# Performance work log

Measured on AMD Instinct MI355X. Metric: run time of the kernel, lower is better.

The kernel has to match this reference:

```python
import jax, jax.numpy as jnp
import numpy as np

N = 16384
C_IN = 128
C_OUT = 128
S_DIM = 4
P_DIM = 32
K = 16


def setup_inputs() -> dict:
    key = jax.random.key(0)
    ks = jax.random.split(key, 8)
    lim = lambda fan_in: 1.0 / np.sqrt(fan_in)
    u = lambda k_, shape, b: jax.random.uniform(k_, shape, jnp.float32, -b, b)
    return {
        "x": jax.random.normal(ks[0], (N, C_IN), jnp.float32),
        "Ws": u(ks[1], (S_DIM, C_IN), lim(C_IN)),
        "bs": u(ks[2], (S_DIM,), lim(C_IN)),
        "Wh": u(ks[3], (P_DIM, C_IN), lim(C_IN)),
        "bh": u(ks[4], (P_DIM,), lim(C_IN)),
        "W1": u(ks[5], (C_OUT, C_IN), lim(C_IN)),
        "W2": u(ks[6], (C_OUT, 2 * P_DIM), lim(2 * P_DIM)),
        "b2": u(ks[7], (C_OUT,), lim(2 * P_DIM)),
        "k": K,
    }


def reference(x, Ws, bs, Wh, bh, W1, W2, b2, k):
    # latent space positions and message vectors
    s = x @ Ws.T + bs            # [N, S]
    h = x @ Wh.T + bh            # [N, P]
    # squared-distance matrix via Gram trick (monotone in true distance,
    # so k-NN indices match torch.cdist + topk(largest=False))
    sq = jnp.sum(s * s, axis=-1)                         # [N]
    d2 = sq[:, None] + sq[None, :] - 2.0 * (s @ s.T)     # [N, N]
    _, idx = jax.lax.top_k(-d2, k)                       # [N, k] neighbour ids (incl. self)
    # exact squared latent distance to selected neighbours (as in torch code)
    s_j = s[idx]                                          # [N, k, S]
    w = jnp.exp(-10.0 * jnp.sum((s[:, None, :] - s_j) ** 2, axis=-1))  # [N, k]
    msg = h[idx] * w[..., None]                           # [N, k, P]
    agg = jnp.concatenate([msg.mean(axis=1), msg.max(axis=1)], axis=-1)  # [N, 2P]
    return x @ W1.T + agg @ W2.T + b2                     # [N, C_OUT]
```

## Files before the change

kernel.cpp:

```cpp
#include <hip/hip_runtime.h>
#include <hip/hip_bf16.h>


#define NPTS 16384
#define CIN  128
#define SD   4
#define PD   32
#define KNN  16
#define COUT 128
#define FLTMAX 3.4028234663852886e+38f
#define NBIN 33
#define QPB  8
#define QCAP 512
#define MCAP 128
#define EPAD 1e-3f

typedef float v2f __attribute__((ext_vector_type(2)));
typedef unsigned int uint;
typedef unsigned long long u64;
typedef unsigned short u16;
typedef __attribute__((ext_vector_type(8))) short bf16x8;
typedef __attribute__((ext_vector_type(4))) float f32x4;
typedef __attribute__((ext_vector_type(16))) float f32x16;

#define WS_S4     0
#define WS_H      0x40000
#define WS_AGG_M  0x280000
#define WS_SA     0x280000
#define WS_SB     0x300000
#define WS_WT_M   0x680000
#define WS_T2     0x6A0000
#define WS_MASK   0x700000
#define WS_NEED_M 0x2700000
#define WS_CJ_F   0x400000
#define WS_AGG_F  0xC00000
#define WS_WT_F   0x1000000
#define JS   16
#define TJF  (NPTS/JS)

__device__ __forceinline__ float d2f(const float4 a, const float4 b) {
  v2f d0 = {a.x - b.x, a.y - b.y};
  v2f d1 = {a.z - b.z, a.w - b.w};
  v2f pr = d0*d0 + d1*d1;
  return pr.x + pr.y;
}

__device__ __forceinline__ u16 f2bf(float x) {
  uint u = __float_as_uint(x);
  uint r = (u + 0x7FFFu + ((u >> 16) & 1u)) >> 16;
  return (u16)r;
}
__device__ __forceinline__ float bf2f(u16 h) {
  return __uint_as_float(((uint)h) << 16);
}

__global__ __launch_bounds__(256) void k1_proj(
    const float* __restrict__ x, const float* __restrict__ Ws, const float* __restrict__ bs,
    const float* __restrict__ Wh, const float* __restrict__ bh,
    float4* __restrict__ s4, float* __restrict__ h) {
  __shared__ float  lw[36*128];
  __shared__ float  lx[64*132];
  __shared__ double rs[3*64*5];
  __shared__ float  rh[3*64*33];
  const int t = threadIdx.x;
  const int row0 = blockIdx.x * 64;
  for (int i2 = t; i2 < 36*128; i2 += 256)
    lw[i2] = (i2 < 512) ? Ws[i2] : Wh[i2 - 512];
#pragma unroll
  for (int g = 0; g < 8; ++g) {
    int fi = g*256 + t;
    int r = fi >> 5, c4 = fi & 31;
    *(float4*)&lx[r*132 + c4*4] = *(const float4*)&x[(size_t)(row0 + r)*CIN + c4*4];
  }
  __syncthreads();
  const int kq = t >> 6;
  const int r  = t & 63;
  const int kb = kq * 32;
  double sacc[4] = {0.0, 0.0, 0.0, 0.0};
  float  hacc[32];
#pragma unroll
  for (int p = 0; p < 32; ++p) hacc[p] = 0.f;
#pragma unroll
  for (int k4 = 0; k4 < 8; ++k4) {
    float4 xv = *(const float4*)&lx[r*132 + kb + k4*4];
    int kg = kb + k4*4;
#pragma unroll
    for (int p = 0; p < 4; ++p) {
      float4 wv = *(const float4*)&lw[p*128 + kg];
      sacc[p] = fma((double)xv.x, (double)wv.x, sacc[p]);
      sacc[p] = fma((double)xv.y, (double)wv.y, sacc[p]);
      sacc[p] = fma((double)xv.z, (double)wv.z, sacc[p]);
      sacc[p] = fma((double)xv.w, (double)wv.w, sacc[p]);
    }
#pragma unroll
    for (int p = 0; p < 32; ++p) {
      float4 wv = *(const float4*)&lw[(4+p)*128 + kg];
      hacc[p] = fmaf(xv.x, wv.x, fmaf(xv.y, wv.y, fmaf(xv.z, wv.z, fmaf(xv.w, wv.w, hacc[p]))));
    }
  }
  if (kq > 0) {
    const int bq = kq - 1;
#pragma unroll
    for (int d = 0; d < 4; ++d) rs[(bq*64 + r)*5 + d] = sacc[d];
#pragma unroll
    for (int p = 0; p < 32; ++p) rh[(bq*64 + r)*33 + p] = hacc[p];
  }
  __syncthreads();
  if (kq == 0) {
    const int row = row0 + r;
    float so[4];
#pragma unroll
    for (int d = 0; d < 4; ++d) {
      double sd = sacc[d] + rs[(0*64 + r)*5 + d] + rs[(1*64 + r)*5 + d]
                + rs[(2*64 + r)*5 + d] + (double)bs[d];
      so[d] = (float)sd;
    }
    s4[row] = make_float4(so[0], so[1], so[2], so[3]);
#pragma unroll
    for (int p4 = 0; p4 < 8; ++p4) {
      float o[4];
#pragma unroll
      for (int c = 0; c < 4; ++c) {
        int p = p4*4 + c;
        o[c] = hacc[p] + rh[(0*64 + r)*33 + p] + rh[(1*64 + r)*33 + p]
             + rh[(2*64 + r)*33 + p] + bh[p];
      }
      *(float4*)&h[(size_t)row*PD + p4*4] = make_float4(o[0], o[1], o[2], o[3]);
    }
  }
}

__global__ __launch_bounds__(256) void k2t_thresh(
    const float4* __restrict__ s4, float* __restrict__ t2) {
  __shared__ float4 tile[2064];
  __shared__ uint   lhist[256*NBIN];
  const int t = threadIdx.x;
#pragma unroll
  for (int g = 0; g < 8; ++g) {
    int j = g*256 + t;
    tile[j + (j >> 7)] = s4[j];
  }
#pragma unroll
  for (int b = 0; b < NBIN; ++b) lhist[t*NBIN + b] = 0u;
  const int ql = t >> 4, tq = t & 15;
  const int q  = blockIdx.x*16 + ql;
  const float4 sq = s4[q];
  __syncthreads();
  float tau = d2f(sq, tile[tq*129]);
#pragma unroll
  for (int m = 1; m < 16; m <<= 1) tau = fmaxf(tau, __shfl_xor(tau, m, 16));
  const int ktop = (int)(__float_as_uint(tau) >> 21);
  const int hb = t*NBIN;
#pragma unroll 4
  for (int u = 0; u < 128; ++u) {
    float4 p = tile[tq*129 + u];
    float e = d2f(sq, p);
    int key = (int)(__float_as_uint(e) >> 21);
    int rel = ktop - key;
    rel = rel < 0 ? 0 : (rel > 32 ? 32 : rel);
    atomicAdd(&lhist[hb + rel], 1u);
  }
  __syncthreads();
  uint c0 = 0, c1 = 0;
  const int qb = ql*16;
  for (int u = 0; u < 16; ++u) {
    c0 += lhist[(qb + u)*NBIN + tq*2];
    c1 += (tq*2 + 1 < NBIN) ? lhist[(qb + u)*NBIN + tq*2 + 1] : 0u;
  }
  int S = (int)(c0 + c1);
#pragma unroll
  for (int d = 1; d < 16; d <<= 1) {
    int v = __shfl_down(S, d, 16);
    S += (tq + d < 16) ? v : 0;
  }
  int g = -1;
  if (S >= KNN) g = 2*tq;
  if (S - (int)c0 >= KNN) g = 2*tq + 1;
#pragma unroll
  for (int m = 1; m < 16; m <<= 1) g = max(g, __shfl_xor(g, m, 16));
  if (tq == 0) {
    uint K = (uint)(ktop - g);
    t2[q] = __uint_as_float((K << 21) | 0x1FFFFFu);
  }
}

__global__ __launch_bounds__(256) void k1b_pack(
    const float4* __restrict__ s4, const float* __restrict__ t2,
    uint4* __restrict__ sA, uint4* __restrict__ sB) {
  const int i = blockIdx.x*256 + threadIdx.x;
  const float4 s = s4[i];
  float sv[4] = {s.x, s.y, s.z, s.w};
  const float n2 = s.x*s.x + s.y*s.y + s.z*s.z + s.w*s.w;
  u16 hb[4], lb[4];
#pragma unroll
  for (int d = 0; d < 4; ++d) {
    u16 hh = f2bf(sv[d]);
    hb[d] = hh;
    lb[d] = f2bf(sv[d] - bf2f(hh));
  }
  const float aq = -0.5f*(n2 - t2[i]) + EPAD;
  const float bn = -0.5f*n2;
  u16 aqh = f2bf(aq); u16 aql = f2bf(aq - bf2f(aqh));
  u16 bnh = f2bf(bn); u16 bnl = f2bf(bn - bf2f(bnh));
  const uint oneone = 0x3F803F80u;
  uint a0 = (uint)hb[0] | ((uint)hb[1] << 16);
  uint a1 = (uint)hb[2] | ((uint)hb[3] << 16);
  uint l0 = (uint)lb[0] | ((uint)lb[1] << 16);
  uint l1 = (uint)lb[2] | ((uint)lb[3] << 16);
  uint aqw = (uint)aqh | ((uint)aql << 16);
  uint bnw = (uint)bnh | ((uint)bnl << 16);
  uint4 A0; A0.x = a0; A0.y = a1; A0.z = a0; A0.w = a1;
  uint4 A1; A1.x = l0; A1.y = l1; A1.z = oneone; A1.w = aqw;
  uint4 B0; B0.x = a0; B0.y = a1; B0.z = l0; B0.w = l1;
  uint4 B1; B1.x = a0; B1.y = a1; B1.z = bnw; B1.w = oneone;
  sA[(size_t)i*2]     = A0;
  sA[(size_t)i*2 + 1] = A1;
  sB[(size_t)i*2]     = B0;
  sB[(size_t)i*2 + 1] = B1;
}

__device__ __forceinline__ uint packbits16(const f32x16 a, const int shft) {
  uint b[4];
#pragma unroll
  for (int g = 0; g < 4; ++g) {
    uint bg = 0u;
#pragma unroll
    for (int e = 3; e >= 0; --e)
      bg = bg + bg + ((~__float_as_uint(a[4*g + e])) >> 31);
    b[g] = bg;
  }
  return (b[0] | (b[1] << 8) | (b[2] << 16) | (b[3] << 24)) << shft;
}

__global__ __launch_bounds__(256) void k2b_mfma(
    const u16* __restrict__ sA, const u16* __restrict__ sB, uint4* __restrict__ maskw) {
  __shared__ u16 lB[1024*16];
  const int t   = threadIdx.x;
  const int wv  = t >> 6, ln = t & 63;
  const int l31 = ln & 31, hi = ln >> 5;
  const int qbase = (blockIdx.x >> 4) * 256 + wv * 64;
  const int j0    = (blockIdx.x & 15) * 1024;
  for (int r = t; r < 1024; r += 256) {
    const uint4* src = (const uint4*)&sB[(size_t)(j0 + r)*16];
    uint4 v0 = src[0], v1 = src[1];
    *(uint4*)&lB[r*16]     = v0;
    *(uint4*)&lB[r*16 + 8] = v1;
  }
  const bf16x8 qf0 = *(const bf16x8*)&sA[(size_t)(qbase + l31)*16 + hi*8];
  const bf16x8 qf1 = *(const bf16x8*)&sA[(size_t)(qbase + 32 + l31)*16 + hi*8];
  __syncthreads();
  const int sh = hi * 4;
  const f32x16 zc = {0.f,0.f,0.f,0.f,0.f,0.f,0.f,0.f,0.f,0.f,0.f,0.f,0.f,0.f,0.f,0.f};
#pragma unroll 1
  for (int cc = 0; cc < 8; ++cc) {
    uint w0[4], w1[4];
#pragma unroll
    for (int jt = 0; jt < 4; ++jt) {
      const bf16x8 af = *(const bf16x8*)&lB[(cc*128 + jt*32 + l31)*16 + hi*8];
      f32x16 a0 = __builtin_amdgcn_mfma_f32_32x32x16_bf16(af, qf0, zc, 0, 0, 0);
      f32x16 a1 = __builtin_amdgcn_mfma_f32_32x32x16_bf16(af, qf1, zc, 0, 0, 0);
      w0[jt] = packbits16(a0, sh);
      w1[jt] = packbits16(a1, sh);
    }
    uint of[4];
#pragma unroll
    for (int jt = 0; jt < 4; ++jt) {
      uint f0 = w0[jt] | (uint)__shfl_xor((int)w0[jt], 32);
      uint f1 = w1[jt] | (uint)__shfl_xor((int)w1[jt], 32);
      of[jt] = hi ? f1 : f0;
    }
    const int c = (blockIdx.x & 15)*8 + cc;
    uint4 o; o.x = of[0]; o.y = of[1]; o.z = of[2]; o.w = of[3];
    maskw[(size_t)c*NPTS + qbase + ln] = o;
  }
}

__global__ __launch_bounds__(256) void k3_sel2(
    const float4* __restrict__ s4, const float* __restrict__ h,
    const uint4* __restrict__ maskw, float* __restrict__ agg) {
  __shared__ u64  qbuf[QPB*MCAP];
  __shared__ u64  keys[QPB*QCAP];
  __shared__ u64  win[QPB*KNN];
  __shared__ uint hist[QPB*32];
  __shared__ uint cnts[QPB];
  __shared__ uint mc[QPB];
  unsigned short* jl = (unsigned short*)qbuf;
  const int t  = threadIdx.x;
  const int ql = t >> 5, ln = t & 31;
  const int q  = blockIdx.x*QPB + ql;
  if (ln == 0) { cnts[ql] = 0u; mc[ql] = 0u; }
  hist[ql*32 + ln] = 0u;
  if (ln < KNN) win[ql*KNN + ln] = 0ull;
  const float4 sq = s4[q];
  __syncthreads();
  const int qa = t & 7;
  const int cg = t >> 3;
  uint wv[16]; int pc = 0;
#pragma unroll
  for (int u = 0; u < 4; ++u) {
    const int c = cg + u*32;
    uint4 m4 = maskw[(size_t)c*NPTS + blockIdx.x*QPB + qa];
    wv[u*4+0] = m4.x; wv[u*4+1] = m4.y; wv[u*4+2] = m4.z; wv[u*4+3] = m4.w;
    pc += __popc(m4.x) + __popc(m4.y) + __popc(m4.z) + __popc(m4.w);
  }
  int base = (int)atomicAdd(&cnts[qa], (uint)pc);
#pragma unroll
  for (int w = 0; w < 16; ++w) {
    uint bits = wv[w];
    const int jb = (cg + (w >> 2)*32)*128 + (w & 3)*32;
    while (bits) {
      int b = __builtin_ctz(bits); bits &= bits - 1;
      if (base < QCAP) jl[qa*QCAP + base] = (unsigned short)(jb + b);
      ++base;
    }
  }
  __syncthreads();
  const int cnt = min((int)cnts[ql], QCAP);
  uint kmax = 0u;
  for (int u = ln; u < cnt; u += 32) {
    int j = jl[ql*QCAP + u];
    float e = d2f(sq, s4[j]);
    uint db = __float_as_uint(e);
    keys[ql*QCAP + u] = ((u64)db << 14) | (uint)j;
    kmax = max(kmax, db >> 21);
  }
#pragma unroll
  for (int m = 1; m < 32; m <<= 1) kmax = max(kmax, (uint)__shfl_xor((int)kmax, m, 32));
  for (int u = ln; u < cnt; u += 32) {
    uint cls = (uint)(keys[ql*QCAP + u] >> 35);
    uint rel = min(kmax - cls, 31u);
    atomicAdd(&hist[ql*32 + rel], 1u);
  }
  __syncthreads();
  uint cum = hist[ql*32 + ln];
#pragma unroll
  for (int d = 1; d < 32; d <<= 1) {
    uint v = (uint)__shfl_down((int)cum, d, 32);
    if (ln + d < 32) cum += v;
  }
  const uint need = (uint)(cnt < KNN ? cnt : KNN);
  u64 bal = __ballot(cum >= need);
  uint half = (uint)(bal >> (((t >> 5) & 1) * 32));
  const uint rstar = 31u - (uint)__builtin_clz(half);
  const uint bcls = kmax - rstar;
  __syncthreads();
  for (int u = ln; u < cnt; u += 32) {
    u64 key = keys[ql*QCAP + u];
    if ((uint)(key >> 35) <= bcls) {
      uint pos = atomicAdd(&mc[ql], 1u);
      if (pos < MCAP) qbuf[ql*MCAP + pos] = key;
    }
  }
  __syncthreads();
  const int mcnt = (int)mc[ql];
  if (mcnt <= MCAP) {
    for (int w = ln; w < mcnt; w += 32) {
      u64 key = qbuf[ql*MCAP + w];
      int rank = 0;
      for (int v = 0; v < mcnt; ++v) rank += (qbuf[ql*MCAP + v] < key) ? 1 : 0;
      if (rank < KNN) win[ql*KNN + rank] = key;
    }
  } else {
    for (int u = ln; u < cnt; u += 32) {
      u64 key = keys[ql*QCAP + u];
      if ((uint)(key >> 35) <= bcls) {
        int rank = 0;
        for (int v = 0; v < cnt; ++v) rank += (keys[ql*QCAP + v] < key) ? 1 : 0;
        if (rank < KNN) win[ql*KNN + rank] = key;
      }
    }
  }
  __syncthreads();
  float sum = 0.f, mx = -FLTMAX;
#pragma unroll 1
  for (int r = 0; r < KNN; ++r) {
    u64 key = win[ql*KNN + r];
    float d2 = __uint_as_float((uint)(key >> 14));
    int j = (int)(key & 16383u);
    float w = __expf(-10.f * d2);
    float m = w * h[(size_t)j*PD + ln];
    sum += m; mx = fmaxf(mx, m);
  }
  agg[(size_t)q*64 + ln]      = sum * 0.0625f;
  agg[(size_t)q*64 + 32 + ln] = mx;
}

__global__ __launch_bounds__(256) void k2_knn_fb(
    const float4* __restrict__ s4, unsigned short* __restrict__ cand_j) {
  __shared__ float4 tile[TJF];
  __shared__ int    lbuf[256*33];
  const int t  = threadIdx.x;
  const int ib = blockIdx.x & 31;
  const int jc = blockIdx.x >> 5;
  const int jbase = jc * TJF;
#pragma unroll
  for (int g = 0; g < 4; ++g) tile[g*256 + t] = s4[jbase + g*256 + t];
  const int ia = ib*256 + t;
  const int ic = ia + 8192;
  const float4 sa = s4[ia];
  const float4 sc = s4[ic];
  __syncthreads();
  float va[KNN], vb[KNN]; int ja[KNN], jb[KNN];
#pragma unroll
  for (int q = 0; q < KNN; ++q) { va[q] = FLTMAX; ja[q] = 0; vb[q] = FLTMAX; jb[q] = 0; }
  float cma = FLTMAX, cmb = FLTMAX;
  int cpa = 0, cpb = 0, ca = 0, cb = 0;
  auto insertA = [&](float e, int jj) {
#pragma unroll
    for (int q = 0; q < KNN; ++q) if (q == cpa) { va[q] = e; ja[q] = jj; }
    cma = va[0]; cpa = 0;
#pragma unroll
    for (int q = 1; q < KNN; ++q) { if (va[q] > cma) { cma = va[q]; cpa = q; } }
  };
  auto insertB = [&](float e, int jj) {
#pragma unroll
    for (int q = 0; q < KNN; ++q) if (q == cpb) { vb[q] = e; jb[q] = jj; }
    cmb = vb[0]; cpb = 0;
#pragma unroll
    for (int q = 1; q < KNN; ++q) { if (vb[q] > cmb) { cmb = vb[q]; cpb = q; } }
  };
  auto compactA = [&]() {
    for (int u = 0; u < ca; ++u) {
      int jj = lbuf[t*33 + u];
      float e = d2f(sa, tile[jj]);
      if (e < cma) insertA(e, jj);
    }
    ca = 0;
  };
  auto compactB = [&]() {
    for (int u = 0; u < cb; ++u) {
      int jj = lbuf[t*33 + 16 + u];
      float e = d2f(sc, tile[jj]);
      if (e < cmb) insertB(e, jj);
    }
    cb = 0;
  };
  for (int ob = 0; ob < TJF/8; ++ob) {
#pragma unroll
    for (int u = 0; u < 8; ++u) {
      int jj = ob*8 + u;
      float4 p = tile[jj];
      float ea = d2f(sa, p);
      float eb = d2f(sc, p);
      if (ea < cma) { lbuf[t*33 + ca] = jj; ++ca; }
      if (eb < cmb) { lbuf[t*33 + 16 + cb] = jj; ++cb; }
    }
    if (__any(ca > 8)) compactA();
    if (__any(cb > 8)) compactB();
  }
  compactA(); compactB();
#pragma unroll
  for (int q = 0; q < KNN; ++q) {
    int c = jc*KNN + q;
    cand_j[(size_t)c*NPTS + ia] = (unsigned short)(ja[q] + jbase);
    cand_j[(size_t)c*NPTS + ic] = (unsigned short)(jb[q] + jbase);
  }
}

__global__ __launch_bounds__(256) void k3_merge_fb(
    const float4* __restrict__ s4, const float4* __restrict__ h4,
    const unsigned short* __restrict__ cand_j, float* __restrict__ agg) {
  __shared__ float le[64*67];
  __shared__ int   lj[64*67];
  const int t  = threadIdx.x;
  const int il = t & 63, tq = t >> 6;
  const int i  = blockIdx.x*64 + il;
  const float4 si = s4[i];
  float val[KNN]; int vid[KNN];
#pragma unroll
  for (int q = 0; q < KNN; ++q) { val[q] = FLTMAX; vid[q] = 0; }
  float cmax = FLTMAX; int cpos = 0;
  for (int u = 0; u < 64; ++u) {
    int c = tq*64 + u;
    int j = cand_j[(size_t)c*NPTS + i];
    float e = d2f(si, s4[j]);
    if (e < cmax) {
#pragma unroll
      for (int q = 0; q < KNN; ++q) if (q == cpos) { val[q] = e; vid[q] = j; }
      cmax = val[0]; cpos = 0;
#pragma unroll
      for (int q = 1; q < KNN; ++q) { if (val[q] > cmax) { cmax = val[q]; cpos = q; } }
    }
  }
#pragma unroll
  for (int q = 0; q < KNN; ++q) {
    le[il*67 + tq*16 + q] = val[q];
    lj[il*67 + tq*16 + q] = vid[q];
  }
  __syncthreads();
  if (t < 64) {
    float mv[KNN]; int mj[KNN];
#pragma unroll
    for (int q = 0; q < KNN; ++q) { mv[q] = FLTMAX; mj[q] = 0; }
    float cm2 = FLTMAX; int cp2 = 0;
    for (int u = 0; u < 64; ++u) {
      float e = le[t*67 + u];
      int   j = lj[t*67 + u];
      if (e < cm2) {
#pragma unroll
        for (int q = 0; q < KNN; ++q) if (q == cp2) { mv[q] = e; mj[q] = j; }
        cm2 = mv[0]; cp2 = 0;
#pragma unroll
        for (int q = 1; q < KNN; ++q) { if (mv[q] > cm2) { cm2 = mv[q]; cp2 = q; } }
      }
    }
#pragma unroll
    for (int q = 0; q < KNN; ++q) {
      le[t*67 + q] = __expf(-10.f * mv[q]);
      lj[t*67 + q] = mj[q];
    }
  }
  __syncthreads();
  float ms[8], mm[8];
#pragma unroll
  for (int p = 0; p < 8; ++p) { ms[p] = 0.f; mm[p] = -FLTMAX; }
#pragma unroll 1
  for (int q = 0; q < KNN; ++q) {
    float w = le[il*67 + q];
    int   j = lj[il*67 + q];
    float4 a = h4[(size_t)j*8 + tq*2];
    float4 b = h4[(size_t)j*8 + tq*2 + 1];
    float m0 = a.x*w, m1 = a.y*w, m2 = a.z*w, m3 = a.w*w;
    float m4 = b.x*w, m5 = b.y*w, m6 = b.z*w, m7 = b.w*w;
    ms[0] += m0; mm[0] = fmaxf(mm[0], m0);
    ms[1] += m1; mm[1] = fmaxf(mm[1], m1);
    ms[2] += m2; mm[2] = fmaxf(mm[2], m2);
    ms[3] += m3; mm[3] = fmaxf(mm[3], m3);
    ms[4] += m4; mm[4] = fmaxf(mm[4], m4);
    ms[5] += m5; mm[5] = fmaxf(mm[5], m5);
    ms[6] += m6; mm[6] = fmaxf(mm[6], m6);
    ms[7] += m7; mm[7] = fmaxf(mm[7], m7);
  }
  float4 o0 = make_float4(ms[0]*0.0625f, ms[1]*0.0625f, ms[2]*0.0625f, ms[3]*0.0625f);
  float4 o1 = make_float4(ms[4]*0.0625f, ms[5]*0.0625f, ms[6]*0.0625f, ms[7]*0.0625f);
  *(float4*)&agg[(size_t)i*64 + tq*8]      = o0;
  *(float4*)&agg[(size_t)i*64 + tq*8 + 4]  = o1;
  *(float4*)&agg[(size_t)i*64 + 32 + tq*8]     = make_float4(mm[0], mm[1], mm[2], mm[3]);
  *(float4*)&agg[(size_t)i*64 + 32 + tq*8 + 4] = make_float4(mm[4], mm[5], mm[6], mm[7]);
}

__global__ __launch_bounds__(256) void k4a_wt(
    const float* __restrict__ W1, const float* __restrict__ W2, float* __restrict__ wT) {
  int idx = blockIdx.x*256 + threadIdx.x;
  if (idx >= 192*COUT) return;
  int k = idx >> 7, c = idx & 127;
  float v = (k < 128) ? W1[(size_t)c*128 + k] : W2[(size_t)c*64 + (k - 128)];
  wT[(size_t)k*COUT + c] = v;
}

__global__ __launch_bounds__(256) void k4_out2(
    const float* __restrict__ x, const float* __restrict__ agg,
    const float* __restrict__ wT, const float* __restrict__ b2,
    float* __restrict__ out) {
  __shared__ float xa[32*192];
  const int t = threadIdx.x;
  const int row0 = blockIdx.x * 32;
#pragma unroll
  for (int g = 0; g < 4; ++g) {
    int fi = g*256 + t;
    int r = fi >> 5, c4 = fi & 31;
    *(float4*)&xa[r*192 + c4*4] = *(const float4*)&x[(size_t)(row0+r)*CIN + c4*4];
  }
#pragma unroll
  for (int g = 0; g < 2; ++g) {
    int fi = g*256 + t;
    int r = fi >> 4, c4 = fi & 15;
    *(float4*)&xa[r*192 + 128 + c4*4] = *(const float4*)&agg[(size_t)(row0+r)*64 + c4*4];
  }
  __syncthreads();
  const int c4 = t & 31;
  const int rg = t >> 5;
  float acc[4][4];
#pragma unroll
  for (int r = 0; r < 4; ++r) { acc[r][0]=0.f; acc[r][1]=0.f; acc[r][2]=0.f; acc[r][3]=0.f; }
  for (int k = 0; k < 192; k += 4) {
    float4 w0 = *(const float4*)&wT[(size_t)(k+0)*COUT + c4*4];
    float4 w1 = *(const float4*)&wT[(size_t)(k+1)*COUT + c4*4];
    float4 w2 = *(const float4*)&wT[(size_t)(k+2)*COUT + c4*4];
    float4 w3 = *(const float4*)&wT[(size_t)(k+3)*COUT + c4*4];
#pragma unroll
    for (int r = 0; r < 4; ++r) {
      float4 xv = *(const float4*)&xa[(rg*4 + r)*192 + k];
      acc[r][0] = fmaf(xv.x, w0.x, fmaf(xv.y, w1.x, fmaf(xv.z, w2.x, fmaf(xv.w, w3.x, acc[r][0]))));
      acc[r][1] = fmaf(xv.x, w0.y, fmaf(xv.y, w1.y, fmaf(xv.z, w2.y, fmaf(xv.w, w3.y, acc[r][1]))));
      acc[r][2] = fmaf(xv.x, w0.z, fmaf(xv.y, w1.z, fmaf(xv.z, w2.z, fmaf(xv.w, w3.z, acc[r][2]))));
      acc[r][3] = fmaf(xv.x, w0.w, fmaf(xv.y, w1.w, fmaf(xv.z, w2.w, fmaf(xv.w, w3.w, acc[r][3]))));
    }
  }
  float4 bias = *(const float4*)&b2[c4*4];
#pragma unroll
  for (int r = 0; r < 4; ++r) {
    float4 o = make_float4(acc[r][0]+bias.x, acc[r][1]+bias.y, acc[r][2]+bias.z, acc[r][3]+bias.w);
    *(float4*)&out[(size_t)(row0 + rg*4 + r)*COUT + c4*4] = o;
  }
}

extern "C" void kernel_launch(void* const* d_in, const int* in_sizes, int n_in,
                              void* d_out, int out_size, void* d_ws, size_t ws_size,
                              hipStream_t stream) {
  const float* x  = (const float*)d_in[0];
  const float* Ws = (const float*)d_in[1];
  const float* bs = (const float*)d_in[2];
  const float* Wh = (const float*)d_in[3];
  const float* bh = (const float*)d_in[4];
  const float* W1 = (const float*)d_in[5];
  const float* W2 = (const float*)d_in[6];
  const float* b2 = (const float*)d_in[7];
  float* out = (float*)d_out;

  char* ws = (char*)d_ws;
  float4* s4 = (float4*)(ws + WS_S4);
  float*  h  = (float*) (ws + WS_H);

  k1_proj<<<NPTS/64, 256, 0, stream>>>(x, Ws, bs, Wh, bh, s4, h);

  if (ws_size >= (size_t)WS_NEED_M) {
    float* t2  = (float*)(ws + WS_T2);
    float* agg = (float*)(ws + WS_AGG_M);
    float* wT  = (float*)(ws + WS_WT_M);
    uint4* sa  = (uint4*)(ws + WS_SA);
    uint4* sb  = (uint4*)(ws + WS_SB);
    uint4* mw  = (uint4*)(ws + WS_MASK);
    k2t_thresh<<<NPTS/16, 256, 0, stream>>>(s4, t2);
    k1b_pack<<<NPTS/256, 256, 0, stream>>>(s4, t2, sa, sb);
    k2b_mfma<<<1024, 256, 0, stream>>>((const u16*)sa, (const u16*)sb, mw);
    k3_sel2<<<NPTS/QPB, 256, 0, stream>>>(s4, h, (const uint4*)mw, agg);
    k4a_wt<<<(192*COUT + 255)/256, 256, 0, stream>>>(W1, W2, wT);
    k4_out2<<<NPTS/32, 256, 0, stream>>>(x, agg, wT, b2, out);
  } else {
    unsigned short* cj = (unsigned short*)(ws + WS_CJ_F);
    float* agg = (float*)(ws + WS_AGG_F);
    float* wT  = (float*)(ws + WS_WT_F);
    k2_knn_fb<<<512, 256, 0, stream>>>(s4, cj);
    k3_merge_fb<<<NPTS/64, 256, 0, stream>>>(s4, (const float4*)h, cj, agg);
    k4a_wt<<<(192*COUT + 255)/256, 256, 0, stream>>>(W1, W2, wT);
    k4_out2<<<NPTS/32, 256, 0, stream>>>(x, agg, wT, b2, out);
  }
}
```

Measured before the change: 207.9 us.

## Fuse MFMA candidate masking with per-thread top-k selection, merge partial lists

Replaces the bitmask-writing MFMA kernel and the separate histogram-based selection kernel with one kernel. Each thread keeps a register top-16 over the candidates from a quarter of the points, and a small merge kernel combines the four partial lists and computes the aggregates. This removes the large mask write and reread and the shared-memory histogram and rank passes. In exchange it launches only 512 blocks of 128 threads, holds 16 64-bit keys per thread in registers, and runs a branchy per-candidate insertion loop.

```diff
diff --git a/kernel.cpp b/kernel.cpp
--- a/kernel.cpp
+++ b/kernel.cpp
@@ -10,9 +10,6 @@
 #define COUT 128
 #define FLTMAX 3.4028234663852886e+38f
 #define NBIN 33
-#define QPB  8
-#define QCAP 512
-#define MCAP 128
 #define EPAD 1e-3f
 
 typedef float v2f __attribute__((ext_vector_type(2)));
@@ -20,7 +17,6 @@
 typedef unsigned long long u64;
 typedef unsigned short u16;
 typedef __attribute__((ext_vector_type(8))) short bf16x8;
-typedef __attribute__((ext_vector_type(4))) float f32x4;
 typedef __attribute__((ext_vector_type(16))) float f32x16;
 
 #define WS_S4     0
@@ -30,7 +26,7 @@
 #define WS_SB     0x300000
 #define WS_WT_M   0x680000
 #define WS_T2     0x6A0000
-#define WS_MASK   0x700000
+#define WS_PW     0x700000
 #define WS_NEED_M 0x2700000
 #define WS_CJ_F   0x400000
 #define WS_AGG_F  0xC00000
@@ -232,157 +228,139 @@
   return (b[0] | (b[1] << 8) | (b[2] << 16) | (b[3] << 24)) << shft;
 }
 
-__global__ __launch_bounds__(256) void k2b_mfma(
-    const u16* __restrict__ sA, const u16* __restrict__ sB, uint4* __restrict__ maskw) {
-  __shared__ u16 lB[1024*16];
+__global__ __launch_bounds__(128) void k2sel(
+    const u16* __restrict__ sA, const u16* __restrict__ sB,
+    const float4* __restrict__ s4, u64* __restrict__ pw) {
+  __shared__ u16    lB[1024*16];
+  __shared__ float4 ls4[1024];
   const int t   = threadIdx.x;
   const int wv  = t >> 6, ln = t & 63;
   const int l31 = ln & 31, hi = ln >> 5;
-  const int qbase = (blockIdx.x >> 4) * 256 + wv * 64;
-  const int j0    = (blockIdx.x & 15) * 1024;
-  for (int r = t; r < 1024; r += 256) {
-    const uint4* src = (const uint4*)&sB[(size_t)(j0 + r)*16];
-    uint4 v0 = src[0], v1 = src[1];
-    *(uint4*)&lB[r*16]     = v0;
-    *(uint4*)&lB[r*16 + 8] = v1;
-  }
-  const bf16x8 qf0 = *(const bf16x8*)&sA[(size_t)(qbase + l31)*16 + hi*8];
-  const bf16x8 qf1 = *(const bf16x8*)&sA[(size_t)(qbase + 32 + l31)*16 + hi*8];
-  __syncthreads();
+  const int qg  = blockIdx.x >> 2, jq = blockIdx.x & 3;
+  const int qwb = qg*128 + wv*64;
+  const int j0  = jq*4096;
+  const int q   = qwb + ln;
+  const float4 sq = s4[q];
+  const bf16x8 qf0 = *(const bf16x8*)&sA[(size_t)(qwb + l31)*16 + hi*8];
+  const bf16x8 qf1 = *(const bf16x8*)&sA[(size_t)(qwb + 32 + l31)*16 + hi*8];
+  u64 kv[16];
+#pragma unroll
+  for (int r = 0; r < 16; ++r) kv[r] = ~0ull;
+  u64 cmx = ~0ull; int cpos = 0;
   const int sh = hi * 4;
   const f32x16 zc = {0.f,0.f,0.f,0.f,0.f,0.f,0.f,0.f,0.f,0.f,0.f,0.f,0.f,0.f,0.f,0.f};
 #pragma unroll 1
-  for (int cc = 0; cc < 8; ++cc) {
-    uint w0[4], w1[4];
-#pragma unroll
-    for (int jt = 0; jt < 4; ++jt) {
-      const bf16x8 af = *(const bf16x8*)&lB[(cc*128 + jt*32 + l31)*16 + hi*8];
-      f32x16 a0 = __builtin_amdgcn_mfma_f32_32x32x16_bf16(af, qf0, zc, 0, 0, 0);
-      f32x16 a1 = __builtin_amdgcn_mfma_f32_32x32x16_bf16(af, qf1, zc, 0, 0, 0);
-      w0[jt] = packbits16(a0, sh);
-      w1[jt] = packbits16(a1, sh);
-    }
-    uint of[4];
-#pragma unroll
-    for (int jt = 0; jt < 4; ++jt) {
-      uint f0 = w0[jt] | (uint)__shfl_xor((int)w0[jt], 32);
-      uint f1 = w1[jt] | (uint)__shfl_xor((int)w1[jt], 32);
-      of[jt] = hi ? f1 : f0;
-    }
-    const int c = (blockIdx.x & 15)*8 + cc;
-    uint4 o; o.x = of[0]; o.y = of[1]; o.z = of[2]; o.w = of[3];
-    maskw[(size_t)c*NPTS + qbase + ln] = o;
-  }
-}
-
-__global__ __launch_bounds__(256) void k3_sel2(
-    const float4* __restrict__ s4, const float* __restrict__ h,
-    const uint4* __restrict__ maskw, float* __restrict__ agg) {
-  __shared__ u64  qbuf[QPB*MCAP];
-  __shared__ u64  keys[QPB*QCAP];
-  __shared__ u64  win[QPB*KNN];
-  __shared__ uint hist[QPB*32];
-  __shared__ uint cnts[QPB];
-  __shared__ uint mc[QPB];
-  unsigned short* jl = (unsigned short*)qbuf;
+  for (int cc = 0; cc < 4; ++cc) {
+    __syncthreads();
+    for (int r = t; r < 1024; r += 128) {
+      const uint4* src = (const uint4*)&sB[(size_t)(j0 + cc*1024 + r)*16];
+      uint4 v0 = src[0], v1 = src[1];
+      *(uint4*)&lB[r*16]     = v0;
+      *(uint4*)&lB[r*16 + 8] = v1;
+      ls4[r] = s4[j0 + cc*1024 + r];
+    }
+    __syncthreads();
+#pragma unroll 1
+    for (int c8 = 0; c8 < 8; ++c8) {
+      uint w0[4], w1[4];
+#pragma unroll
+      for (int jt = 0; jt < 4; ++jt) {
+        const bf16x8 af = *(const bf16x8*)&lB[(c8*128 + jt*32 + l31)*16 + hi*8];
+        f32x16 a0 = __builtin_amdgcn_mfma_f32_32x32x16_bf16(af, qf0, zc, 0, 0, 0);
+        f32x16 a1 = __builtin_amdgcn_mfma_f32_32x32x16_bf16(af, qf1, zc, 0, 0, 0);
+        w0[jt] = packbits16(a0, sh);
+        w1[jt] = packbits16(a1, sh);
+      }
+#pragma unroll
+      for (int jt = 0; jt < 4; ++jt) {
+        uint f0 = w0[jt] | (uint)__shfl_xor((int)w0[jt], 32);
+        uint f1 = w1[jt] | (uint)__shfl_xor((int)w1[jt], 32);
+        uint bits = hi ? f1 : f0;
+        while (bits) {
+          int b = __builtin_ctz(bits); bits &= bits - 1;
+          const int jl = c8*128 + jt*32 + b;
+          float4 p = ls4[jl];
+          float e = d2f(sq, p);
+          u64 key = ((u64)__float_as_uint(e) << 14) | (uint)(j0 + cc*1024 + jl);
+          if (key < cmx) {
+#pragma unroll
+            for (int r16 = 0; r16 < 16; ++r16) if (r16 == cpos) kv[r16] = key;
+            cmx = kv[0]; cpos = 0;
+#pragma unroll
+            for (int r16 = 1; r16 < 16; ++r16) { if (kv[r16] > cmx) { cmx = kv[r16]; cpos = r16; } }
+          }
+        }
+      }
+    }
+  }
+#pragma unroll
+  for (int r = 0; r < 16; ++r)
+    pw[(size_t)(jq*16 + r)*NPTS + q] = kv[r];
+}
+
+__global__ __launch_bounds__(256) void k3m(
+    const u64* __restrict__ pw, const float4* __restrict__ h4, float* __restrict__ agg) {
+  __shared__ u64   lk[64*65];
+  __shared__ float le[64*17];
+  __shared__ int   lj[64*17];
   const int t  = threadIdx.x;
-  const int ql = t >> 5, ln = t & 31;
-  const int q  = blockIdx.x*QPB + ql;
-  if (ln == 0) { cnts[ql] = 0u; mc[ql] = 0u; }
-  hist[ql*32 + ln] = 0u;
-  if (ln < KNN) win[ql*KNN + ln] = 0ull;
-  const float4 sq = s4[q];
-  __syncthreads();
-  const int qa = t & 7;
-  const int cg = t >> 3;
-  uint wv[16]; int pc = 0;
-#pragma unroll
-  for (int u = 0; u < 4; ++u) {
-    const int c = cg + u*32;
-    uint4 m4 = maskw[(size_t)c*NPTS + blockIdx.x*QPB + qa];
-    wv[u*4+0] = m4.x; wv[u*4+1] = m4.y; wv[u*4+2] = m4.z; wv[u*4+3] = m4.w;
-    pc += __popc(m4.x) + __popc(m4.y) + __popc(m4.z) + __popc(m4.w);
-  }
-  int base = (int)atomicAdd(&cnts[qa], (uint)pc);
-#pragma unroll
-  for (int w = 0; w < 16; ++w) {
-    uint bits = wv[w];
-    const int jb = (cg + (w >> 2)*32)*128 + (w & 3)*32;
-    while (bits) {
-      int b = __builtin_ctz(bits); bits &= bits - 1;
-      if (base < QCAP) jl[qa*QCAP + base] = (unsigned short)(jb + b);
-      ++base;
-    }
-  }
-  __syncthreads();
-  const int cnt = min((int)cnts[ql], QCAP);
-  uint kmax = 0u;
-  for (int u = ln; u < cnt; u += 32) {
-    int j = jl[ql*QCAP + u];
-    float e = d2f(sq, s4[j]);
-    uint db = __float_as_uint(e);
-    keys[ql*QCAP + u] = ((u64)db << 14) | (uint)j;
-    kmax = max(kmax, db >> 21);
-  }
-#pragma unroll
-  for (int m = 1; m < 32; m <<= 1) kmax = max(kmax, (uint)__shfl_xor((int)kmax, m, 32));
-  for (int u = ln; u < cnt; u += 32) {
-    uint cls = (uint)(keys[ql*QCAP + u] >> 35);
-    uint rel = min(kmax - cls, 31u);
-    atomicAdd(&hist[ql*32 + rel], 1u);
-  }
-  __syncthreads();
-  uint cum = hist[ql*32 + ln];
-#pragma unroll
-  for (int d = 1; d < 32; d <<= 1) {
-    uint v = (uint)__shfl_down((int)cum, d, 32);
-    if (ln + d < 32) cum += v;
-  }
-  const uint need = (uint)(cnt < KNN ? cnt : KNN);
-  u64 bal = __ballot(cum >= need);
-  uint half = (uint)(bal >> (((t >> 5) & 1) * 32));
-  const uint rstar = 31u - (uint)__builtin_clz(half);
-  const uint bcls = kmax - rstar;
-  __syncthreads();
-  for (int u = ln; u < cnt; u += 32) {
-    u64 key = keys[ql*QCAP + u];
-    if ((uint)(key >> 35) <= bcls) {
-      uint pos = atomicAdd(&mc[ql], 1u);
-      if (pos < MCAP) qbuf[ql*MCAP + pos] = key;
-    }
-  }
-  __syncthreads();
-  const int mcnt = (int)mc[ql];
-  if (mcnt <= MCAP) {
-    for (int w = ln; w < mcnt; w += 32) {
-      u64 key = qbuf[ql*MCAP + w];
-      int rank = 0;
-      for (int v = 0; v < mcnt; ++v) rank += (qbuf[ql*MCAP + v] < key) ? 1 : 0;
-      if (rank < KNN) win[ql*KNN + rank] = key;
-    }
-  } else {
-    for (int u = ln; u < cnt; u += 32) {
-      u64 key = keys[ql*QCAP + u];
-      if ((uint)(key >> 35) <= bcls) {
-        int rank = 0;
-        for (int v = 0; v < cnt; ++v) rank += (keys[ql*QCAP + v] < key) ? 1 : 0;
-        if (rank < KNN) win[ql*KNN + rank] = key;
+  const int il = t & 63, tq = t >> 6;
+  const int i  = blockIdx.x*64 + il;
+#pragma unroll
+  for (int u = 0; u < 16; ++u) {
+    const int c = tq*16 + u;
+    lk[il*65 + c] = pw[(size_t)c*NPTS + i];
+  }
+  __syncthreads();
+  if (t < 64) {
+    u64 kv[16];
+#pragma unroll
+    for (int r = 0; r < 16; ++r) kv[r] = ~0ull;
+    u64 cmx = ~0ull; int cpos = 0;
+    for (int u = 0; u < 64; ++u) {
+      u64 key = lk[t*65 + u];
+      if (key < cmx) {
+#pragma unroll
+        for (int r16 = 0; r16 < 16; ++r16) if (r16 == cpos) kv[r16] = key;
+        cmx = kv[0]; cpos = 0;
+#pragma unroll
+        for (int r16 = 1; r16 < 16; ++r16) { if (kv[r16] > cmx) { cmx = kv[r16]; cpos = r16; } }
       }
     }
-  }
-  __syncthreads();
-  float sum = 0.f, mx = -FLTMAX;
+#pragma unroll
+    for (int r = 0; r < 16; ++r) {
+      float d2v = __uint_as_float((uint)(kv[r] >> 14));
+      le[t*17 + r] = __expf(-10.f * d2v);
+      lj[t*17 + r] = (int)(kv[r] & 16383u);
+    }
+  }
+  __syncthreads();
+  float ms[8], mm[8];
+#pragma unroll
+  for (int p = 0; p < 8; ++p) { ms[p] = 0.f; mm[p] = -FLTMAX; }
 #pragma unroll 1
   for (int r = 0; r < KNN; ++r) {
-    u64 key = win[ql*KNN + r];
-    float d2 = __uint_as_float((uint)(key >> 14));
-    int j = (int)(key & 16383u);
-    float w = __expf(-10.f * d2);
-    float m = w * h[(size_t)j*PD + ln];
-    sum += m; mx = fmaxf(mx, m);
-  }
-  agg[(size_t)q*64 + ln]      = sum * 0.0625f;
-  agg[(size_t)q*64 + 32 + ln] = mx;
+    float w = le[il*17 + r];
+    int   j = lj[il*17 + r];
+    float4 a = h4[(size_t)j*8 + tq*2];
+    float4 b = h4[(size_t)j*8 + tq*2 + 1];
+    float m0 = a.x*w, m1 = a.y*w, m2 = a.z*w, m3 = a.w*w;
+    float m4 = b.x*w, m5 = b.y*w, m6 = b.z*w, m7 = b.w*w;
+    ms[0] += m0; mm[0] = fmaxf(mm[0], m0);
+    ms[1] += m1; mm[1] = fmaxf(mm[1], m1);
+    ms[2] += m2; mm[2] = fmaxf(mm[2], m2);
+    ms[3] += m3; mm[3] = fmaxf(mm[3], m3);
+    ms[4] += m4; mm[4] = fmaxf(mm[4], m4);
+    ms[5] += m5; mm[5] = fmaxf(mm[5], m5);
+    ms[6] += m6; mm[6] = fmaxf(mm[6], m6);
+    ms[7] += m7; mm[7] = fmaxf(mm[7], m7);
+  }
+  float4 o0 = make_float4(ms[0]*0.0625f, ms[1]*0.0625f, ms[2]*0.0625f, ms[3]*0.0625f);
+  float4 o1 = make_float4(ms[4]*0.0625f, ms[5]*0.0625f, ms[6]*0.0625f, ms[7]*0.0625f);
+  *(float4*)&agg[(size_t)i*64 + tq*8]      = o0;
+  *(float4*)&agg[(size_t)i*64 + tq*8 + 4]  = o1;
+  *(float4*)&agg[(size_t)i*64 + 32 + tq*8]     = make_float4(mm[0], mm[1], mm[2], mm[3]);
+  *(float4*)&agg[(size_t)i*64 + 32 + tq*8 + 4] = make_float4(mm[4], mm[5], mm[6], mm[7]);
 }
 
 __global__ __launch_bounds__(256) void k2_knn_fb(
@@ -620,11 +598,11 @@
     float* wT  = (float*)(ws + WS_WT_M);
     uint4* sa  = (uint4*)(ws + WS_SA);
     uint4* sb  = (uint4*)(ws + WS_SB);
-    uint4* mw  = (uint4*)(ws + WS_MASK);
+    u64*   pw  = (u64*)  (ws + WS_PW);
     k2t_thresh<<<NPTS/16, 256, 0, stream>>>(s4, t2);
     k1b_pack<<<NPTS/256, 256, 0, stream>>>(s4, t2, sa, sb);
-    k2b_mfma<<<1024, 256, 0, stream>>>((const u16*)sa, (const u16*)sb, mw);
-    k3_sel2<<<NPTS/QPB, 256, 0, stream>>>(s4, h, (const uint4*)mw, agg);
+    k2sel<<<512, 128, 0, stream>>>((const u16*)sa, (const u16*)sb, s4, pw);
+    k3m<<<NPTS/64, 256, 0, stream>>>(pw, (const float4*)h, agg);
     k4a_wt<<<(192*COUT + 255)/256, 256, 0, stream>>>(W1, W2, wT);
     k4_out2<<<NPTS/32, 256, 0, stream>>>(x, agg, wT, b2, out);
   } else {
```

Result: slower. 347.2 us (+67.0%).
